# Optimization experiments

Hardware: AMD Instinct MI355X
Metric: run time of the kernel (lower is better)

## Reference

```python
import jax, jax.numpy as jnp
import numpy as np
from jax import lax

B, C, H, W = 2, 128, 96, 96
K = 3
KK = K * K
EPS = 1e-5


def setup_inputs() -> dict:
    key = jax.random.key(0)
    ks = jax.random.split(key, 4)
    d = {"hu": jax.random.normal(ks[0], (B, C, H, W), jnp.float32)}
    for i in range(3):
        k = jax.random.split(ks[i + 1], 7)
        d["off_w%d" % (i + 1)] = jax.random.normal(k[0], (3 * KK, C, K, K), jnp.float32) * 0.01
        d["off_b%d" % (i + 1)] = jax.random.normal(k[1], (3 * KK,), jnp.float32) * 0.01
        d["w%d" % (i + 1)] = jax.random.normal(k[2], (C, C, K, K), jnp.float32) / np.float32(np.sqrt(C * KK))
        d["g%d" % (i + 1)] = jax.random.uniform(k[3], (C,), jnp.float32) + 0.5
        d["b%d" % (i + 1)] = jax.random.normal(k[4], (C,), jnp.float32) * 0.1
        d["m%d" % (i + 1)] = jax.random.normal(k[5], (C,), jnp.float32) * 0.1
        d["v%d" % (i + 1)] = jax.random.uniform(k[6], (C,), jnp.float32) + 0.5
    return d


def _mod_deform_conv(x, w, offset, mask, dilation):
    # x: [B,C,H,W]; offset: [B,2*KK,H,W] (dy,dx interleaved per kernel tap);
    # mask: [B,KK,H,W] (already sigmoid'ed). Zero padding outside the image.
    Hh, Ww = x.shape[2], x.shape[3]
    pad = dilation * (K - 1) // 2
    ky = jnp.repeat(jnp.arange(K), K).astype(x.dtype)  # [KK] row of each tap
    kx = jnp.tile(jnp.arange(K), K).astype(x.dtype)    # [KK] col of each tap
    gy = (jnp.arange(Hh, dtype=x.dtype) - pad)[None, :, None] + (ky * dilation)[:, None, None]  # [KK,H,1]
    gx = (jnp.arange(Ww, dtype=x.dtype) - pad)[None, None, :] + (kx * dilation)[:, None, None]  # [KK,1,W]
    off = offset.reshape(x.shape[0], KK, 2, Hh, Ww)
    py = gy[None] + off[:, :, 0]  # [B,KK,H,W] sampling row
    px = gx[None] + off[:, :, 1]  # [B,KK,H,W] sampling col

    def sample_one(xb, pyb, pxb, mb):
        # xb: [C,H,W]; pyb/pxb/mb: [KK,H,W]
        y0 = jnp.floor(pyb)
        x0 = jnp.floor(pxb)
        ly = pyb - y0
        lx = pxb - x0
        acc = jnp.zeros((xb.shape[0],) + pyb.shape, xb.dtype)
        for dy, wy in ((0, 1.0 - ly), (1, ly)):
            for dx, wx in ((0, 1.0 - lx), (1, lx)):
                yi = y0 + dy
                xi = x0 + dx
                valid = (yi >= 0) & (yi <= Hh - 1) & (xi >= 0) & (xi <= Ww - 1)
                yc = jnp.clip(yi, 0, Hh - 1).astype(jnp.int32)
                xc = jnp.clip(xi, 0, Ww - 1).astype(jnp.int32)
                v = xb[:, yc, xc]  # gather -> [C,KK,H,W]
                acc = acc + v * (wy * wx * valid.astype(xb.dtype))[None]
        return acc * mb[None]  # modulation

    sampled = jax.vmap(sample_one)(x, py, px, mask)  # [B,C,KK,H,W]
    return jnp.einsum('bckhw,ock->bohw', sampled, w.reshape(w.shape[0], w.shape[1], KK))


def _block(x, off_w, off_b, w, g, b, m, v, dilation):
    pad = dilation * (K - 1) // 2
    om = lax.conv_general_dilated(
        x, off_w, (1, 1), [(pad, pad), (pad, pad)],
        rhs_dilation=(dilation, dilation),
        dimension_numbers=('NCHW', 'OIHW', 'NCHW')) + off_b[None, :, None, None]
    offset = om[:, :2 * KK]
    mask = jax.nn.sigmoid(om[:, 2 * KK:])
    y = _mod_deform_conv(x, w, offset, mask, dilation)
    scale = (g / jnp.sqrt(v + EPS))[None, :, None, None]  # BN (inference form)
    y = (y - m[None, :, None, None]) * scale + b[None, :, None, None]
    return jax.nn.relu(y)


def reference(hu, off_w1, off_b1, w1, g1, b1, m1, v1,
              off_w2, off_b2, w2, g2, b2, m2, v2,
              off_w3, off_b3, w3, g3, b3, m3, v3):
    a1 = _block(hu, off_w1, off_b1, w1, g1, b1, m1, v1, 2) + hu
    a2 = _block(a1, off_w2, off_b2, w2, g2, b2, m2, v2, 4) + a1
    a3 = _block(a2, off_w3, off_b3, w3, g3, b3, m3, v3, 8) + a2
    return a3
```

## Files before the change

### kernel.cpp

```cpp
#include <hip/hip_runtime.h>
#include <math.h>

constexpr int Bn  = 2;
constexpr int Cn  = 128;
constexpr int Hn  = 96;
constexpr int Wn  = 96;
constexpr int HWn = Hn * Wn;
constexpr int CHWn = Cn * HWn;
constexpr int KCn = Cn * 9;
constexpr float EPSn = 1e-5f;
constexpr int KPAD = 1160;

typedef short bf16x8 __attribute__((ext_vector_type(8)));
typedef float f32x4  __attribute__((ext_vector_type(4)));

static __device__ inline short f2bf(float f) {
    union { float f; unsigned u; } v; v.f = f;
    unsigned r = v.u + 0x7fff + ((v.u >> 16) & 1);
    return (short)(r >> 16);
}
static __device__ inline unsigned pack2(float a, float b) {
    unsigned r;
    asm("v_cvt_pk_bf16_f32 %0, %1, %2" : "=v"(r) : "v"(a), "v"(b));
    return r;
}

__global__ __launch_bounds__(256) void cvt_w_shuf(
    const float* __restrict__ w, short* __restrict__ wbs)
{
    int t = blockIdx.x * 256 + threadIdx.x;
    if (t >= Cn * KCn) return;
    int e = t & 7, l = (t >> 3) & 63, rest = t >> 9;
    int j = rest % 36, wv = rest / 36;
    int lr = l & 15, lq = l >> 4;
    int o = wv * 16 + lr;
    int kidx = j * 32 + lq * 8 + e;
    int k = kidx >> 7, c = kidx & 127;
    wbs[t] = f2bf(w[o * KCn + c * 9 + k]);
}

__global__ __launch_bounds__(256) void cvt_ow_shuf(
    const float* __restrict__ ow, short* __restrict__ owbs)
{
    int t = blockIdx.x * 256 + threadIdx.x;
    if (t >= 32 * KCn) return;
    int e = t & 7, l = (t >> 3) & 63, rest = t >> 9;
    int kk = rest % 9, wv = rest / 9;
    int mh = wv & 1, ks = wv >> 1;
    int lr = l & 15, lq = l >> 4;
    int o = mh * 16 + lr;
    int kidx = ks * 288 + kk * 32 + lq * 8 + e;
    int k = kidx >> 7, c = kidx & 127;
    owbs[t] = (o < 27) ? f2bf(ow[o * KCn + c * 9 + k]) : (short)0;
}

__global__ __launch_bounds__(256) void nchw2nhwc(
    const float* __restrict__ x, float* __restrict__ xTf,
    unsigned short* __restrict__ xTb)
{
    __shared__ float Tl[128][65];
    const int t = threadIdx.x;
    const int pix0 = blockIdx.x * 64;
    const int b   = pix0 / HWn;
    const int sp0 = pix0 - b * HWn;
    const float* xb = x + b * CHWn + sp0 + (t & 63);
    const int c0 = t >> 6;
#pragma unroll 8
    for (int i = 0; i < 32; ++i) {
        const int c = c0 + 4 * i;
        Tl[c][t & 63] = xb[c * HWn];
    }
    __syncthreads();
    float* dstf = xTf + pix0 * 128;
    unsigned short* dstb = xTb + pix0 * 128;
#pragma unroll 8
    for (int i = 0; i < 32; ++i) {
        const int o = t + 256 * i;
        float v = Tl[o & 127][o >> 7];
        dstf[o] = v;
        dstb[o] = (unsigned short)f2bf(v);
    }
}

__global__ __launch_bounds__(512, 6) void fused_stage(
    const unsigned short* __restrict__ xTb, const float* __restrict__ xTf,
    const short* __restrict__ wbs, const short* __restrict__ owbs,
    const float* __restrict__ obv,
    const float* __restrict__ gv, const float* __restrict__ bv,
    const float* __restrict__ mv, const float* __restrict__ vv,
    float* __restrict__ outTf, unsigned short* __restrict__ outTb,
    float* __restrict__ outC, int dil, int last)
{
    __shared__ short S[16 * KPAD];
    __shared__ float offL[16][18];
    __shared__ float maskL[16][9];

    const int t   = threadIdx.x;
    const int l   = t & 63;
    const int wv  = t >> 6;
    const int lh  = l >> 5;
    const int lc  = l & 31;

    const int bid = blockIdx.x;
    const int swz = (bid & 7) * 144 + (bid >> 3);
    const int pix0 = swz * 16;
    const int b   = pix0 / HWn;
    const int sp0 = pix0 - b * HWn;
    const int hy  = sp0 / Wn;
    const int wx0 = sp0 - hy * Wn;
    const int basep = b * HWn;

#pragma unroll
    for (int bch = 0; bch < 3; ++bch) {
        uint2 vle[3];
#pragma unroll
        for (int u = 0; u < 3; ++u) {
            const int k  = bch * 3 + u;
            const int pp = wv * 2 + lh;
            const int iy = hy + (k / 3 - 1) * dil;
            const int ix = wx0 + pp + (k % 3 - 1) * dil;
            const bool v = (iy >= 0) && (iy < Hn) && (ix >= 0) && (ix < Wn);
            const int aof = v ? (basep + iy * Wn + ix) : basep;
            uint2 val = ((const uint2*)(xTb + aof * 128))[lc];
            vle[u].x = v ? val.x : 0u;
            vle[u].y = v ? val.y : 0u;
        }
#pragma unroll
        for (int u = 0; u < 3; ++u) {
            const int k  = bch * 3 + u;
            const int pp = wv * 2 + lh;
            ((uint2*)&S[pp * KPAD + k * 128])[lc] = vle[u];
        }
    }
    __syncthreads();

    f32x4 oacc = {0.f, 0.f, 0.f, 0.f};
    {
        const short* oarow = owbs + (wv * 9) * 512 + l * 8;
        const int ks = wv >> 1;
        const short* srow  = &S[(l & 15) * KPAD + ks * 288 + ((l >> 4) * 8)];
#pragma unroll
        for (int bch = 0; bch < 3; ++bch) {
            bf16x8 af[3], bf[3];
#pragma unroll
            for (int u = 0; u < 3; ++u) af[u] = *(const bf16x8*)(oarow + (bch * 3 + u) * 512);
#pragma unroll
            for (int u = 0; u < 3; ++u) bf[u] = *(const bf16x8*)(srow  + (bch * 3 + u) * 32);
#pragma unroll
            for (int u = 0; u < 3; ++u)
                oacc = __builtin_amdgcn_mfma_f32_16x16x32_bf16(af[u], bf[u], oacc, 0, 0, 0);
        }
    }
    __syncthreads();
    float* red = (float*)S;
    *(f32x4*)&red[wv * 256 + l * 4] = oacc;
    __syncthreads();
    if (wv < 2) {
        f32x4 s0 = *(const f32x4*)&red[(0 * 2 + wv) * 256 + l * 4];
        f32x4 s1 = *(const f32x4*)&red[(1 * 2 + wv) * 256 + l * 4];
        f32x4 s2 = *(const f32x4*)&red[(2 * 2 + wv) * 256 + l * 4];
        f32x4 s3 = *(const f32x4*)&red[(3 * 2 + wv) * 256 + l * 4];
        f32x4 sm = (s0 + s1) + (s2 + s3);
#pragma unroll
        for (int r = 0; r < 4; ++r) {
            int oc = wv * 16 + ((l >> 4) << 2) + r;
            if (oc < 18) {
                offL[l & 15][oc] = sm[r] + obv[oc];
            } else if (oc < 27) {
                float z = sm[r] + obv[oc];
                maskL[l & 15][oc - 18] = 1.f / (1.f + expf(-z));
            }
        }
    }
    __syncthreads();

    int pw0i = 0, pw1i = 0, pw2i = 0, pw3i = 0, pa0 = 0, pa1 = 0, pdx = 0;
    if (l < 18) {
        const int p = wv * 2 + l / 9;
        const int k = l - 9 * (l / 9);
        const float offy = offL[p][2 * k];
        const float offx = offL[p][2 * k + 1];
        const float m    = maskL[p][k];
        const float py = (float)(hy + (k / 3 - 1) * dil) + offy;
        const float px = (float)(wx0 + p + (k % 3 - 1) * dil) + offx;
        const float y0f = floorf(py), x0f = floorf(px);
        const float ly = py - y0f, lx = px - x0f;
        const int y0 = (int)y0f, x0 = (int)x0f;
        const float yv0 = (y0 >= 0 && y0 < Hn)      ? 1.f : 0.f;
        const float yv1 = (y0 >= -1 && y0 < Hn - 1) ? 1.f : 0.f;
        const float xv0 = (x0 >= 0 && x0 < Wn)      ? 1.f : 0.f;
        const float xv1 = (x0 >= -1 && x0 < Wn - 1) ? 1.f : 0.f;
        const float wy0 = (1.f - ly) * yv0 * m;
        const float wy1 = ly * yv1 * m;
        const float wxa = (1.f - lx) * xv0;
        const float wxb = lx * xv1;
        pw0i = __float_as_int(wy0 * wxa);
        pw1i = __float_as_int(wy0 * wxb);
        pw2i = __float_as_int(wy1 * wxa);
        pw3i = __float_as_int(wy1 * wxb);
        const int y0c = min(max(y0, 0), Hn - 1), y1c = min(max(y0 + 1, 0), Hn - 1);
        const int x0c = min(max(x0, 0), Wn - 1), x1c = min(max(x0 + 1, 0), Wn - 1);
        pa0 = (basep + y0c * Wn + x0c) * 128;
        pa1 = (basep + y1c * Wn + x1c) * 128;
        pdx = (x1c - x0c) * 128;
    }

#pragma unroll
    for (int bch = 0; bch < 6; ++bch) {
        unsigned u00[3], u01[3], u10[3], u11[3];
        float    w00[3], w01[3], w10[3], w11[3];
#pragma unroll
        for (int u = 0; u < 3; ++u) {
            const int i = bch * 3 + u;
            w00[u] = __int_as_float(__builtin_amdgcn_readlane(pw0i, i));
            w01[u] = __int_as_float(__builtin_amdgcn_readlane(pw1i, i));
            w10[u] = __int_as_float(__builtin_amdgcn_readlane(pw2i, i));
            w11[u] = __int_as_float(__builtin_amdgcn_readlane(pw3i, i));
            const int a00 = __builtin_amdgcn_readlane(pa0, i);
            const int a11 = __builtin_amdgcn_readlane(pa1, i);
            const int dxk = __builtin_amdgcn_readlane(pdx, i);
            const unsigned short* xp = xTb + a00;
            const unsigned short* xq = xTb + a11;
            u00[u] = ((const unsigned*)xp)[l];
            u01[u] = ((const unsigned*)(xp + dxk))[l];
            u10[u] = ((const unsigned*)(xq - dxk))[l];
            u11[u] = ((const unsigned*)xq)[l];
        }
#pragma unroll
        for (int u = 0; u < 3; ++u) {
            const int i  = bch * 3 + u;
            const int di = i / 9;
            const int k  = i - di * 9;
            const int pp = wv * 2 + di;
            const float f00a = __int_as_float(u00[u] << 16);
            const float f00b = __int_as_float(u00[u] & 0xffff0000u);
            const float f01a = __int_as_float(u01[u] << 16);
            const float f01b = __int_as_float(u01[u] & 0xffff0000u);
            const float f10a = __int_as_float(u10[u] << 16);
            const float f10b = __int_as_float(u10[u] & 0xffff0000u);
            const float f11a = __int_as_float(u11[u] << 16);
            const float f11b = __int_as_float(u11[u] & 0xffff0000u);
            float s0 = w00[u] * f00a + w01[u] * f01a + w10[u] * f10a + w11[u] * f11a;
            float s1 = w00[u] * f00b + w01[u] * f01b + w10[u] * f10b + w11[u] * f11b;
            ((unsigned*)&S[pp * KPAD + k * 128])[l] = pack2(s0, s1);
        }
    }
    __syncthreads();

    f32x4 dacc = {0.f, 0.f, 0.f, 0.f};
    {
        const short* darow = wbs + (wv * 36) * 512 + l * 8;
        const short* srow  = &S[(l & 15) * KPAD + ((l >> 4) * 8)];
#pragma unroll
        for (int bch = 0; bch < 6; ++bch) {
            bf16x8 af[6], bf[6];
#pragma unroll
            for (int u = 0; u < 6; ++u) af[u] = *(const bf16x8*)(darow + (bch * 6 + u) * 512);
#pragma unroll
            for (int u = 0; u < 6; ++u) bf[u] = *(const bf16x8*)(srow  + (bch * 6 + u) * 32);
#pragma unroll
            for (int u = 0; u < 6; ++u)
                dacc = __builtin_amdgcn_mfma_f32_16x16x32_bf16(af[u], bf[u], dacc, 0, 0, 0);
        }
    }

    const int pp  = l & 15;
    const int ocb = wv * 16 + ((l >> 4) << 2);
    if (last) {
#pragma unroll
        for (int r = 0; r < 4; ++r) {
            const int oc = ocb + r;
            const float sc = gv[oc] * rsqrtf(vv[oc] + EPSn);
            float y = (dacc[r] - mv[oc]) * sc + bv[oc];
            y = fmaxf(y, 0.f);
            y += xTf[(pix0 + pp) * 128 + oc];
            outC[b * CHWn + oc * HWn + sp0 + pp] = y;
        }
    } else {
        __syncthreads();
        float* O = (float*)S;
#pragma unroll
        for (int r = 0; r < 4; ++r) {
            const int oc = ocb + r;
            const float sc = gv[oc] * rsqrtf(vv[oc] + EPSn);
            float y = (dacc[r] - mv[oc]) * sc + bv[oc];
            O[pp * 132 + oc] = fmaxf(y, 0.f);
        }
        __syncthreads();
        const int o  = t * 4;
        const int qp = o >> 7, qc = o & 127;
        f32x4 yv = *(f32x4*)&O[qp * 132 + qc];
        f32x4 rv = *(const f32x4*)&xTf[(pix0 + qp) * 128 + qc];
        yv += rv;
        *(f32x4*)&outTf[(pix0 + qp) * 128 + qc] = yv;
        uint2 pk;
        pk.x = pack2(yv[0], yv[1]);
        pk.y = pack2(yv[2], yv[3]);
        *(uint2*)&outTb[(pix0 + qp) * 128 + qc] = pk;
    }
}

extern "C" void kernel_launch(void* const* d_in, const int* in_sizes, int n_in,
                              void* d_out, int out_size, void* d_ws, size_t ws_size,
                              hipStream_t stream) {
    (void)in_sizes; (void)n_in; (void)out_size; (void)ws_size;

    const float* hu = (const float*)d_in[0];

    short* wbs  = (short*)d_ws;
    short* owbs = wbs + 3 * Cn * KCn;
    unsigned short* T0b = (unsigned short*)(owbs + 3 * 32 * KCn);
    unsigned short* T1b = T0b + Bn * CHWn;
    float* T0f = (float*)(T1b + Bn * CHWn);
    float* T1f = T0f + Bn * CHWn;

    for (int i = 0; i < 3; ++i) {
        cvt_w_shuf<<<(Cn * KCn + 255) / 256, 256, 0, stream>>>(
            (const float*)d_in[3 + 7 * i], wbs + i * Cn * KCn);
        cvt_ow_shuf<<<(32 * KCn + 255) / 256, 256, 0, stream>>>(
            (const float*)d_in[1 + 7 * i], owbs + i * 32 * KCn);
    }

    nchw2nhwc<<<(Bn * HWn) / 64, 256, 0, stream>>>(hu, T0f, T0b);

    const int dils[3] = {2, 4, 8};
    const unsigned short* insb[3] = {T0b, T1b, T0b};
    const float*          insf[3] = {T0f, T1f, T0f};
    float*          outsf[3] = {T1f, T0f, nullptr};
    unsigned short* outsb[3] = {T1b, T0b, nullptr};
    const int nblk = (Bn * HWn) / 16;

    for (int i = 0; i < 3; ++i) {
        const float* obv = (const float*)d_in[2 + 7 * i];
        const float* gv  = (const float*)d_in[4 + 7 * i];
        const float* bv  = (const float*)d_in[5 + 7 * i];
        const float* mv  = (const float*)d_in[6 + 7 * i];
        const float* vv  = (const float*)d_in[7 + 7 * i];
        const int last = (i == 2);

        fused_stage<<<nblk, 512, 0, stream>>>(
            insb[i], insf[i], wbs + i * Cn * KCn, owbs + i * 32 * KCn, obv,
            gv, bv, mv, vv, outsf[i], outsb[i],
            last ? (float*)d_out : nullptr, dils[i], last);
    }
}
```

Before: 121.5 us.

## Process 32 pixels per block to reuse weight fragments across two MFMA tiles

Each block of the fused deformable-conv stage now handles 32 pixels instead of 16. Every weight A-fragment loaded from global memory feeds two MFMAs (two 16-pixel tiles), which halves weight traffic per pixel. The offset conv, the bilinear sampling and the epilogue are redistributed across the 8 waves to match. The cost is double the LDS per block, more registers, a lower occupancy hint and half as many blocks.

```diff
diff --git a/kernel.cpp b/kernel.cpp
--- a/kernel.cpp
+++ b/kernel.cpp
@@ -10,6 +10,7 @@
 constexpr int KCn = Cn * 9;
 constexpr float EPSn = 1e-5f;
 constexpr int KPAD = 1160;
+constexpr int PXB  = 32;
 
 typedef short bf16x8 __attribute__((ext_vector_type(8)));
 typedef float f32x4  __attribute__((ext_vector_type(4)));
@@ -45,8 +46,8 @@
     int t = blockIdx.x * 256 + threadIdx.x;
     if (t >= 32 * KCn) return;
     int e = t & 7, l = (t >> 3) & 63, rest = t >> 9;
-    int kk = rest % 9, wv = rest / 9;
-    int mh = wv & 1, ks = wv >> 1;
+    int kk = rest % 9, wvv = rest / 9;
+    int mh = wvv & 1, ks = wvv >> 1;
     int lr = l & 15, lq = l >> 4;
     int o = mh * 16 + lr;
     int kidx = ks * 288 + kk * 32 + lq * 8 + e;
@@ -82,7 +83,7 @@
     }
 }
 
-__global__ __launch_bounds__(512, 6) void fused_stage(
+__global__ __launch_bounds__(512, 4) void fused_stage(
     const unsigned short* __restrict__ xTb, const float* __restrict__ xTf,
     const short* __restrict__ wbs, const short* __restrict__ owbs,
     const float* __restrict__ obv,
@@ -91,19 +92,20 @@
     float* __restrict__ outTf, unsigned short* __restrict__ outTb,
     float* __restrict__ outC, int dil, int last)
 {
-    __shared__ short S[16 * KPAD];
-    __shared__ float offL[16][18];
-    __shared__ float maskL[16][9];
+    __shared__ short S[PXB * KPAD];
+    __shared__ float offL[PXB][18];
+    __shared__ float maskL[PXB][9];
 
     const int t   = threadIdx.x;
     const int l   = t & 63;
     const int wv  = t >> 6;
     const int lh  = l >> 5;
     const int lc  = l & 31;
+    const int lr  = l & 15, lq = l >> 4;
 
     const int bid = blockIdx.x;
-    const int swz = (bid & 7) * 144 + (bid >> 3);
-    const int pix0 = swz * 16;
+    const int swz = (bid & 7) * 72 + (bid >> 3);
+    const int pix0 = swz * PXB;
     const int b   = pix0 / HWn;
     const int sp0 = pix0 - b * HWn;
     const int hy  = sp0 / Wn;
@@ -111,12 +113,14 @@
     const int basep = b * HWn;
 
 #pragma unroll
-    for (int bch = 0; bch < 3; ++bch) {
+    for (int bch = 0; bch < 6; ++bch) {
         uint2 vle[3];
 #pragma unroll
         for (int u = 0; u < 3; ++u) {
-            const int k  = bch * 3 + u;
-            const int pp = wv * 2 + lh;
+            const int it = bch * 3 + u;
+            const int k  = it % 9;
+            const int pi = it / 9;
+            const int pp = wv * 4 + pi * 2 + lh;
             const int iy = hy + (k / 3 - 1) * dil;
             const int ix = wx0 + pp + (k % 3 - 1) * dil;
             const bool v = (iy >= 0) && (iy < Hn) && (ix >= 0) && (ix < Wn);
@@ -127,18 +131,22 @@
         }
 #pragma unroll
         for (int u = 0; u < 3; ++u) {
-            const int k  = bch * 3 + u;
-            const int pp = wv * 2 + lh;
+            const int it = bch * 3 + u;
+            const int k  = it % 9;
+            const int pi = it / 9;
+            const int pp = wv * 4 + pi * 2 + lh;
             ((uint2*)&S[pp * KPAD + k * 128])[lc] = vle[u];
         }
     }
     __syncthreads();
 
+    const int mh = wv & 1, ph = (wv >> 1) & 1, kh = wv >> 2;
     f32x4 oacc = {0.f, 0.f, 0.f, 0.f};
-    {
-        const short* oarow = owbs + (wv * 9) * 512 + l * 8;
-        const int ks = wv >> 1;
-        const short* srow  = &S[(l & 15) * KPAD + ks * 288 + ((l >> 4) * 8)];
+#pragma unroll
+    for (int ks2 = 0; ks2 < 2; ++ks2) {
+        const int ks = kh * 2 + ks2;
+        const short* oarow = owbs + ((mh + ks * 2) * 9) * 512 + l * 8;
+        const short* srow  = &S[(ph * 16 + lr) * KPAD + ks * 288 + lq * 8];
 #pragma unroll
         for (int bch = 0; bch < 3; ++bch) {
             bf16x8 af[3], bf[3];
@@ -155,28 +163,27 @@
     float* red = (float*)S;
     *(f32x4*)&red[wv * 256 + l * 4] = oacc;
     __syncthreads();
-    if (wv < 2) {
-        f32x4 s0 = *(const f32x4*)&red[(0 * 2 + wv) * 256 + l * 4];
-        f32x4 s1 = *(const f32x4*)&red[(1 * 2 + wv) * 256 + l * 4];
-        f32x4 s2 = *(const f32x4*)&red[(2 * 2 + wv) * 256 + l * 4];
-        f32x4 s3 = *(const f32x4*)&red[(3 * 2 + wv) * 256 + l * 4];
-        f32x4 sm = (s0 + s1) + (s2 + s3);
+    if (wv < 4) {
+        f32x4 s0 = *(const f32x4*)&red[wv * 256 + l * 4];
+        f32x4 s1 = *(const f32x4*)&red[(wv + 4) * 256 + l * 4];
+        f32x4 sm = s0 + s1;
+        const int px = (wv >> 1) * 16 + lr;
 #pragma unroll
         for (int r = 0; r < 4; ++r) {
-            int oc = wv * 16 + ((l >> 4) << 2) + r;
+            int oc = (wv & 1) * 16 + lq * 4 + r;
             if (oc < 18) {
-                offL[l & 15][oc] = sm[r] + obv[oc];
+                offL[px][oc] = sm[r] + obv[oc];
             } else if (oc < 27) {
                 float z = sm[r] + obv[oc];
-                maskL[l & 15][oc - 18] = 1.f / (1.f + expf(-z));
+                maskL[px][oc - 18] = 1.f / (1.f + expf(-z));
             }
         }
     }
     __syncthreads();
 
     int pw0i = 0, pw1i = 0, pw2i = 0, pw3i = 0, pa0 = 0, pa1 = 0, pdx = 0;
-    if (l < 18) {
-        const int p = wv * 2 + l / 9;
+    if (l < 36) {
+        const int p = wv * 4 + l / 9;
         const int k = l - 9 * (l / 9);
         const float offy = offL[p][2 * k];
         const float offx = offL[p][2 * k + 1];
@@ -206,7 +213,7 @@
     }
 
 #pragma unroll
-    for (int bch = 0; bch < 6; ++bch) {
+    for (int bch = 0; bch < 12; ++bch) {
         unsigned u00[3], u01[3], u10[3], u11[3];
         float    w00[3], w01[3], w10[3], w11[3];
 #pragma unroll
@@ -231,7 +238,7 @@
             const int i  = bch * 3 + u;
             const int di = i / 9;
             const int k  = i - di * 9;
-            const int pp = wv * 2 + di;
+            const int pp = wv * 4 + di;
             const float f00a = __int_as_float(u00[u] << 16);
             const float f00b = __int_as_float(u00[u] & 0xffff0000u);
             const float f01a = __int_as_float(u01[u] << 16);
@@ -247,56 +254,74 @@
     }
     __syncthreads();
 
-    f32x4 dacc = {0.f, 0.f, 0.f, 0.f};
+    f32x4 dacc0 = {0.f, 0.f, 0.f, 0.f}, dacc1 = {0.f, 0.f, 0.f, 0.f};
     {
         const short* darow = wbs + (wv * 36) * 512 + l * 8;
-        const short* srow  = &S[(l & 15) * KPAD + ((l >> 4) * 8)];
+        const short* srow0 = &S[lr * KPAD + lq * 8];
+        const short* srow1 = &S[(16 + lr) * KPAD + lq * 8];
 #pragma unroll
         for (int bch = 0; bch < 6; ++bch) {
-            bf16x8 af[6], bf[6];
-#pragma unroll
-            for (int u = 0; u < 6; ++u) af[u] = *(const bf16x8*)(darow + (bch * 6 + u) * 512);
-#pragma unroll
-            for (int u = 0; u < 6; ++u) bf[u] = *(const bf16x8*)(srow  + (bch * 6 + u) * 32);
-#pragma unroll
-            for (int u = 0; u < 6; ++u)
-                dacc = __builtin_amdgcn_mfma_f32_16x16x32_bf16(af[u], bf[u], dacc, 0, 0, 0);
-        }
-    }
-
-    const int pp  = l & 15;
-    const int ocb = wv * 16 + ((l >> 4) << 2);
+            bf16x8 af[6], bf0[6], bf1[6];
+#pragma unroll
+            for (int u = 0; u < 6; ++u) af[u]  = *(const bf16x8*)(darow + (bch * 6 + u) * 512);
+#pragma unroll
+            for (int u = 0; u < 6; ++u) bf0[u] = *(const bf16x8*)(srow0 + (bch * 6 + u) * 32);
+#pragma unroll
+            for (int u = 0; u < 6; ++u) bf1[u] = *(const bf16x8*)(srow1 + (bch * 6 + u) * 32);
+#pragma unroll
+            for (int u = 0; u < 6; ++u) {
+                dacc0 = __builtin_amdgcn_mfma_f32_16x16x32_bf16(af[u], bf0[u], dacc0, 0, 0, 0);
+                dacc1 = __builtin_amdgcn_mfma_f32_16x16x32_bf16(af[u], bf1[u], dacc1, 0, 0, 0);
+            }
+        }
+    }
+
+    const int ocb = wv * 16 + (lq << 2);
     if (last) {
 #pragma unroll
-        for (int r = 0; r < 4; ++r) {
-            const int oc = ocb + r;
-            const float sc = gv[oc] * rsqrtf(vv[oc] + EPSn);
-            float y = (dacc[r] - mv[oc]) * sc + bv[oc];
-            y = fmaxf(y, 0.f);
-            y += xTf[(pix0 + pp) * 128 + oc];
-            outC[b * CHWn + oc * HWn + sp0 + pp] = y;
+        for (int pf = 0; pf < 2; ++pf) {
+            const f32x4 dv = pf ? dacc1 : dacc0;
+            const int px = pf * 16 + lr;
+#pragma unroll
+            for (int r = 0; r < 4; ++r) {
+                const int oc = ocb + r;
+                const float sc = gv[oc] * rsqrtf(vv[oc] + EPSn);
+                float y = (dv[r] - mv[oc]) * sc + bv[oc];
+                y = fmaxf(y, 0.f);
+                y += xTf[(pix0 + px) * 128 + oc];
+                outC[b * CHWn + oc * HWn + sp0 + px] = y;
+            }
         }
     } else {
         __syncthreads();
         float* O = (float*)S;
 #pragma unroll
-        for (int r = 0; r < 4; ++r) {
-            const int oc = ocb + r;
-            const float sc = gv[oc] * rsqrtf(vv[oc] + EPSn);
-            float y = (dacc[r] - mv[oc]) * sc + bv[oc];
-            O[pp * 132 + oc] = fmaxf(y, 0.f);
+        for (int pf = 0; pf < 2; ++pf) {
+            const f32x4 dv = pf ? dacc1 : dacc0;
+            const int px = pf * 16 + lr;
+            f32x4 y;
+#pragma unroll
+            for (int r = 0; r < 4; ++r) {
+                const int oc = ocb + r;
+                const float sc = gv[oc] * rsqrtf(vv[oc] + EPSn);
+                y[r] = fmaxf((dv[r] - mv[oc]) * sc + bv[oc], 0.f);
+            }
+            *(f32x4*)&O[px * 132 + ocb] = y;
         }
         __syncthreads();
-        const int o  = t * 4;
-        const int qp = o >> 7, qc = o & 127;
-        f32x4 yv = *(f32x4*)&O[qp * 132 + qc];
-        f32x4 rv = *(const f32x4*)&xTf[(pix0 + qp) * 128 + qc];
-        yv += rv;
-        *(f32x4*)&outTf[(pix0 + qp) * 128 + qc] = yv;
-        uint2 pk;
-        pk.x = pack2(yv[0], yv[1]);
-        pk.y = pack2(yv[2], yv[3]);
-        *(uint2*)&outTb[(pix0 + qp) * 128 + qc] = pk;
+#pragma unroll
+        for (int it = 0; it < 2; ++it) {
+            const int o  = t * 4 + it * 2048;
+            const int qp = o >> 7, qc = o & 127;
+            f32x4 yv = *(f32x4*)&O[qp * 132 + qc];
+            f32x4 rv = *(const f32x4*)&xTf[(pix0 + qp) * 128 + qc];
+            yv += rv;
+            *(f32x4*)&outTf[(pix0 + qp) * 128 + qc] = yv;
+            uint2 pk;
+            pk.x = pack2(yv[0], yv[1]);
+            pk.y = pack2(yv[2], yv[3]);
+            *(uint2*)&outTb[(pix0 + qp) * 128 + qc] = pk;
+        }
     }
 }
 
@@ -328,7 +353,7 @@
     const float*          insf[3] = {T0f, T1f, T0f};
     float*          outsf[3] = {T1f, T0f, nullptr};
     unsigned short* outsb[3] = {T1b, T0b, nullptr};
-    const int nblk = (Bn * HWn) / 16;
+    const int nblk = (Bn * HWn) / PXB;
 
     for (int i = 0; i < 3; ++i) {
         const float* obv = (const float*)d_in[2 + 7 * i];
```

Measured after the change: 132.2 us. 8.8% more time.
